# Kernel optimization log

Hardware: AMD Instinct MI355X
Metric: run time of the kernel (lower is better)

Reference implementation:

```python
import jax, jax.numpy as jnp
import numpy as np

B, IN, H, OUT, E = 4096, 1024, 2048, 1024, 16

def setup_inputs() -> dict:
    key = jax.random.key(0)
    ks = jax.random.split(key, 8)
    def lin_init(k, shape, fan_in):
        bound = 1.0 / np.sqrt(fan_in)
        return jax.random.uniform(k, shape, jnp.float32, -bound, bound)
    return {
        "obs": jax.random.normal(ks[0], (B, IN), jnp.float32),
        "switch_idx": jax.random.randint(ks[1], (B,), 0, E, jnp.int32),
        "pre_w": lin_init(ks[2], (H, IN), IN),
        "pre_b": lin_init(ks[3], (H,), IN),
        "expert_w": lin_init(ks[4], (E, H, H), H),
        "expert_b": lin_init(ks[5], (E, H), H),
        "post_w": lin_init(ks[6], (OUT, H), H),
        "post_b": lin_init(ks[7], (OUT,), H),
    }

def reference(obs, switch_idx, pre_w, pre_b, expert_w, expert_b, post_w, post_b):
    # pre_switch: Linear + Tanh
    x = jnp.tanh(obs @ pre_w.T + pre_b)                      # [B, H]
    # compute ALL switch experts (faithful to torch.stack over switches)
    all_x = jnp.einsum("bi,eoi->beo", x, expert_w) + expert_b  # [B, E, H]
    # gather the selected expert output per sample
    x = jnp.take_along_axis(all_x, switch_idx[:, None, None].astype(jnp.int32), axis=1)[:, 0]  # [B, H]
    # post_switch: Tanh, Linear, Tanh
    x = jnp.tanh(x)
    return jnp.tanh(x @ post_w.T + post_b)                   # [B, OUT]
```

## Files before the change

### kernel.cpp

```cpp
#include <hip/hip_runtime.h>


#define Bsz 4096
#define INd 1024
#define Hd  2048
#define OUTd 1024
#define NEXP 16

typedef short bf16x8 __attribute__((ext_vector_type(8)));
typedef float f32x4 __attribute__((ext_vector_type(4)));
typedef unsigned short u16;

__device__ __forceinline__ u16 f2bf(float f) {
  unsigned u = __float_as_uint(f);
  u += 0x7FFF + ((u >> 16) & 1);
  return (u16)(u >> 16);
}

__device__ __forceinline__ float fast_tanh(float x) {
  float ax = fabsf(x);
  float e = __expf(2.0f * ax);
  float t = 1.0f - 2.0f / (e + 1.0f);
  return x < 0.0f ? -t : t;
}

#define GLL16(g, l)                                                            \
  __builtin_amdgcn_global_load_lds(                                            \
      (const __attribute__((address_space(1))) unsigned int*)(g),              \
      (__attribute__((address_space(3))) unsigned int*)(l), 16, 0, 0)

__device__ __forceinline__ void stage128(const u16* gbase, int ldk, u16* lds, int t) {
  const int row = t >> 3;
  const int gc8 = ((t & 7) ^ (row & 7)) << 3;
#pragma unroll
  for (int p = 0; p < 4; ++p)
    GLL16(gbase + (size_t)(row + 32 * p) * ldk + gc8, lds + ((t + 256 * p) << 3));
}

__device__ __forceinline__ void stage64(const u16* gbase, int ldk, u16* lds, int t) {
  const int row = t >> 3;
  const int gc8 = ((t & 7) ^ (row & 7)) << 3;
#pragma unroll
  for (int p = 0; p < 2; ++p)
    GLL16(gbase + (size_t)(row + 32 * p) * ldk + gc8, lds + ((t + 256 * p) << 3));
}

__device__ __forceinline__ void stage_gather(const u16* X1k, const int rowg[4],
                                             const u16* zeroc, u16* lds, int t) {
  const int gc8 = ((t & 7) ^ ((t >> 3) & 7)) << 3;
#pragma unroll
  for (int p = 0; p < 4; ++p) {
    const u16* g = (rowg[p] >= 0) ? X1k + (size_t)rowg[p] * Hd + gc8 : zeroc;
    GLL16(g, lds + ((t + 256 * p) << 3));
  }
}

struct F32Tile { float4 v[8]; };
__device__ __forceinline__ void loadF32tile(const float* W, int ldk, int t, F32Tile& r) {
  const int brow = t & 127, half = t >> 7;
  const float* p = W + (size_t)brow * ldk + (half << 5);
#pragma unroll
  for (int q = 0; q < 8; ++q) r.v[q] = *(const float4*)(p + 4 * q);
}
__device__ __forceinline__ void writeF32tile(const F32Tile& r, u16* lds, int t) {
  const int brow = t & 127, half = t >> 7;
#pragma unroll
  for (int q2 = 0; q2 < 4; ++q2) {
    const float4 x = r.v[2 * q2], y = r.v[2 * q2 + 1];
    bf16x8 o;
    o[0] = (short)f2bf(x.x); o[1] = (short)f2bf(x.y);
    o[2] = (short)f2bf(x.z); o[3] = (short)f2bf(x.w);
    o[4] = (short)f2bf(y.x); o[5] = (short)f2bf(y.y);
    o[6] = (short)f2bf(y.z); o[7] = (short)f2bf(y.w);
    const int gq = (half << 2) + q2;
    const int c = gq ^ (brow & 7);
    *(bf16x8*)&lds[brow * 64 + (c << 3)] = o;
  }
}

template <int MI>
__device__ __forceinline__ void compute_tile(const u16* As, const u16* Bs,
                                             int wm, int wn, int fr, int fq,
                                             f32x4 (&acc)[MI][4]) {
#pragma unroll
  for (int ks = 0; ks < 2; ++ks) {
    const int ch = (((ks << 2) + fq) ^ (fr & 7)) << 3;
    bf16x8 af[MI], bq[4];
#pragma unroll
    for (int i = 0; i < MI; ++i) af[i] = *(const bf16x8*)&As[(wm + 16 * i + fr) * 64 + ch];
#pragma unroll
    for (int j = 0; j < 4; ++j) bq[j] = *(const bf16x8*)&Bs[(wn + 16 * j + fr) * 64 + ch];
#pragma unroll
    for (int i = 0; i < MI; ++i)
#pragma unroll
      for (int j = 0; j < 4; ++j)
        acc[i][j] = __builtin_amdgcn_mfma_f32_16x16x32_bf16(af[i], bq[j], acc[i][j], 0, 0, 0);
  }
}

__global__ __launch_bounds__(256) void k_bucket(const int* __restrict__ idx,
                                                int* __restrict__ offs,
                                                int* __restrict__ rows,
                                                int* __restrict__ zc) {
  __shared__ int cnt[NEXP];
  __shared__ int base[NEXP];
  int t = threadIdx.x;
  if (t < 16) zc[t] = 0;
  if (t < NEXP) cnt[t] = 0;
  __syncthreads();
  for (int b = t; b < Bsz; b += 256) atomicAdd(&cnt[idx[b]], 1);
  __syncthreads();
  if (t == 0) {
    int s = 0;
    for (int e = 0; e < NEXP; ++e) { base[e] = s; offs[e] = s; s += cnt[e]; }
    offs[NEXP] = s;
  }
  __syncthreads();
  for (int b = t; b < Bsz; b += 256) {
    int e = idx[b];
    int p = atomicAdd(&base[e], 1);
    rows[p] = b;
  }
}

__global__ __launch_bounds__(256) void k_cvt(const float* __restrict__ src,
                                             u16* __restrict__ dst, int n) {
  int i = (blockIdx.x * 256 + threadIdx.x) * 8;
  if (i >= n) return;
  float4 a = *(const float4*)(src + i);
  float4 b = *(const float4*)(src + i + 4);
  bf16x8 o;
  o[0] = (short)f2bf(a.x); o[1] = (short)f2bf(a.y);
  o[2] = (short)f2bf(a.z); o[3] = (short)f2bf(a.w);
  o[4] = (short)f2bf(b.x); o[5] = (short)f2bf(b.y);
  o[6] = (short)f2bf(b.z); o[7] = (short)f2bf(b.w);
  *(bf16x8*)(dst + i) = o;
}

template <bool PC>
__global__ __launch_bounds__(256) void k_pre_t(const float* __restrict__ obs32,
                                               const u16* __restrict__ obsb,
                                               const float* __restrict__ prew32,
                                               const u16* __restrict__ prewb,
                                               const float* __restrict__ pre_b,
                                               u16* __restrict__ X1) {
  __shared__ u16 As[2][128 * 64];
  __shared__ u16 Bs[2][128 * 64];
  const int tid = threadIdx.x, lane = tid & 63, wv = tid >> 6;
  const int wm = (wv >> 1) << 6, wn = (wv & 1) << 6;
  const int fr = lane & 15, fq = lane >> 4;
  const int n0 = blockIdx.x * 128, m0 = blockIdx.y * 128;
  f32x4 acc[4][4] = {};
  const int NT = INd / 64;

  if constexpr (PC) {
    stage128(obsb + (size_t)m0 * INd, INd, As[0], tid);
    stage128(prewb + (size_t)n0 * INd, INd, Bs[0], tid);
    __syncthreads();
    for (int kt = 0; kt < NT; ++kt) {
      const int nb = (kt + 1) & 1;
      if (kt + 1 < NT) {
        stage128(obsb + (size_t)m0 * INd + (kt + 1) * 64, INd, As[nb], tid);
        stage128(prewb + (size_t)n0 * INd + (kt + 1) * 64, INd, Bs[nb], tid);
      }
      compute_tile<4>(As[kt & 1], Bs[kt & 1], wm, wn, fr, fq, acc);
      __syncthreads();
    }
  } else {
    F32Tile ra, rb;
    loadF32tile(obs32 + (size_t)m0 * INd, INd, tid, ra);
    loadF32tile(prew32 + (size_t)n0 * INd, INd, tid, rb);
    writeF32tile(ra, As[0], tid);
    writeF32tile(rb, Bs[0], tid);
    __syncthreads();
    for (int kt = 0; kt < NT; ++kt) {
      const int nb = (kt + 1) & 1;
      const bool more = (kt + 1) < NT;
      F32Tile na, nbv;
      if (more) {
        loadF32tile(obs32 + (size_t)m0 * INd + (kt + 1) * 64, INd, tid, na);
        loadF32tile(prew32 + (size_t)n0 * INd + (kt + 1) * 64, INd, tid, nbv);
      }
      compute_tile<4>(As[kt & 1], Bs[kt & 1], wm, wn, fr, fq, acc);
      if (more) { writeF32tile(na, As[nb], tid); writeF32tile(nbv, Bs[nb], tid); }
      __syncthreads();
    }
  }

#pragma unroll
  for (int j = 0; j < 4; ++j) {
    int col = n0 + wn + 16 * j + fr;
    float bias = pre_b[col];
#pragma unroll
    for (int i = 0; i < 4; ++i) {
      int rb2 = m0 + wm + 16 * i + fq * 4;
#pragma unroll
      for (int r = 0; r < 4; ++r)
        X1[(size_t)(rb2 + r) * Hd + col] = f2bf(fast_tanh(acc[i][j][r] + bias));
    }
  }
}

template <bool PC>
__global__ __launch_bounds__(256) void k_expert_t(const u16* __restrict__ X1,
                                                  const float* __restrict__ ew32,
                                                  const u16* __restrict__ ewb,
                                                  const float* __restrict__ eb,
                                                  const int* __restrict__ offs,
                                                  const int* __restrict__ rows,
                                                  const u16* __restrict__ zeroc,
                                                  u16* __restrict__ Z) {
  const int e = blockIdx.y >> 5, rt = blockIdx.y & 31;
  const int seg = offs[e], cnt = offs[e + 1] - seg;
  const int tbase = rt * 128;
  if (tbase >= cnt) return;
  const int nval = min(128, cnt - tbase);
  const int n0 = blockIdx.x * 128;

  __shared__ u16 As[2][128 * 64];
  __shared__ u16 Bs[2][128 * 64];
  const int tid = threadIdx.x, lane = tid & 63, wv = tid >> 6;
  const int wm = (wv >> 1) << 6, wn = (wv & 1) << 6;
  const int fr = lane & 15, fq = lane >> 4;

  int rowg[4];
  {
    const int r0 = tid >> 3;
#pragma unroll
    for (int p = 0; p < 4; ++p) {
      int ar = r0 + 32 * p;
      rowg[p] = (ar < nval) ? rows[seg + tbase + ar] : -1;
    }
  }
  f32x4 acc[4][4] = {};
  const int NT = Hd / 64;

  if constexpr (PC) {
    const u16* We = ewb + (size_t)e * Hd * Hd + (size_t)n0 * Hd;
    stage_gather(X1, rowg, zeroc, As[0], tid);
    stage128(We, Hd, Bs[0], tid);
    __syncthreads();
    for (int kt = 0; kt < NT; ++kt) {
      const int nb = (kt + 1) & 1;
      if (kt + 1 < NT) {
        stage_gather(X1 + (kt + 1) * 64, rowg, zeroc, As[nb], tid);
        stage128(We + (kt + 1) * 64, Hd, Bs[nb], tid);
      }
      compute_tile<4>(As[kt & 1], Bs[kt & 1], wm, wn, fr, fq, acc);
      __syncthreads();
    }
  } else {
    const float* We32 = ew32 + (size_t)e * Hd * Hd + (size_t)n0 * Hd;
    stage_gather(X1, rowg, zeroc, As[0], tid);
    {
      F32Tile rb;
      loadF32tile(We32, Hd, tid, rb);
      writeF32tile(rb, Bs[0], tid);
    }
    __syncthreads();
    for (int kt = 0; kt < NT; ++kt) {
      const int nb = (kt + 1) & 1;
      const bool more = (kt + 1) < NT;
      F32Tile rn;
      if (more) {
        stage_gather(X1 + (kt + 1) * 64, rowg, zeroc, As[nb], tid);
        loadF32tile(We32 + (kt + 1) * 64, Hd, tid, rn);
      }
      compute_tile<4>(As[kt & 1], Bs[kt & 1], wm, wn, fr, fq, acc);
      if (more) writeF32tile(rn, Bs[nb], tid);
      __syncthreads();
    }
  }

#pragma unroll
  for (int i = 0; i < 4; ++i) {
#pragma unroll
    for (int r = 0; r < 4; ++r) {
      int arow = wm + 16 * i + fq * 4 + r;
      if (arow < nval) {
        int orow = rows[seg + tbase + arow];
#pragma unroll
        for (int j = 0; j < 4; ++j) {
          int col = n0 + wn + 16 * j + fr;
          float bias = eb[(size_t)e * Hd + col];
          Z[(size_t)orow * Hd + col] = f2bf(fast_tanh(acc[i][j][r] + bias));
        }
      }
    }
  }
}

template <bool PC>
__global__ __launch_bounds__(256) void k_post_t(const u16* __restrict__ Z,
                                                const float* __restrict__ pw32,
                                                const u16* __restrict__ pwb,
                                                const float* __restrict__ pb,
                                                float* __restrict__ out) {
  __shared__ u16 As[2][64 * 64];
  __shared__ u16 Bs[2][128 * 64];
  const int tid = threadIdx.x, lane = tid & 63, wv = tid >> 6;
  const int wm = (wv >> 1) << 5, wn = (wv & 1) << 6;
  const int fr = lane & 15, fq = lane >> 4;
  const int n0 = blockIdx.x * 128, m0 = blockIdx.y * 64;
  f32x4 acc[2][4] = {};
  const int NT = Hd / 64;

  if constexpr (PC) {
    stage64(Z + (size_t)m0 * Hd, Hd, As[0], tid);
    stage128(pwb + (size_t)n0 * Hd, Hd, Bs[0], tid);
    __syncthreads();
    for (int kt = 0; kt < NT; ++kt) {
      const int nb = (kt + 1) & 1;
      if (kt + 1 < NT) {
        stage64(Z + (size_t)m0 * Hd + (kt + 1) * 64, Hd, As[nb], tid);
        stage128(pwb + (size_t)n0 * Hd + (kt + 1) * 64, Hd, Bs[nb], tid);
      }
      compute_tile<2>(As[kt & 1], Bs[kt & 1], wm, wn, fr, fq, acc);
      __syncthreads();
    }
  } else {
    stage64(Z + (size_t)m0 * Hd, Hd, As[0], tid);
    {
      F32Tile rb;
      loadF32tile(pw32 + (size_t)n0 * Hd, Hd, tid, rb);
      writeF32tile(rb, Bs[0], tid);
    }
    __syncthreads();
    for (int kt = 0; kt < NT; ++kt) {
      const int nb = (kt + 1) & 1;
      const bool more = (kt + 1) < NT;
      F32Tile rn;
      if (more) {
        stage64(Z + (size_t)m0 * Hd + (kt + 1) * 64, Hd, As[nb], tid);
        loadF32tile(pw32 + (size_t)n0 * Hd + (kt + 1) * 64, Hd, tid, rn);
      }
      compute_tile<2>(As[kt & 1], Bs[kt & 1], wm, wn, fr, fq, acc);
      if (more) writeF32tile(rn, Bs[nb], tid);
      __syncthreads();
    }
  }

#pragma unroll
  for (int j = 0; j < 4; ++j) {
    int col = n0 + wn + 16 * j + fr;
    float bias = pb[col];
#pragma unroll
    for (int i = 0; i < 2; ++i) {
      int rb2 = m0 + wm + 16 * i + fq * 4;
#pragma unroll
      for (int r = 0; r < 4; ++r)
        out[(size_t)(rb2 + r) * OUTd + col] = fast_tanh(acc[i][j][r] + bias);
    }
  }
}

extern "C" void kernel_launch(void* const* d_in, const int* in_sizes, int n_in,
                              void* d_out, int out_size, void* d_ws, size_t ws_size,
                              hipStream_t stream) {
  const float* obs   = (const float*)d_in[0];
  const int*   sw    = (const int*)d_in[1];
  const float* pre_w = (const float*)d_in[2];
  const float* pre_b = (const float*)d_in[3];
  const float* ew    = (const float*)d_in[4];
  const float* eb    = (const float*)d_in[5];
  const float* pw    = (const float*)d_in[6];
  const float* pb    = (const float*)d_in[7];
  float* out = (float*)d_out;

  char* ws = (char*)d_ws;
  int* offs = (int*)ws;
  int* rows = (int*)(ws + 128);
  u16* zeroc = (u16*)(ws + 128 + 16384);
  const size_t MISC = 65536;
  u16* X1     = (u16*)(ws + MISC);
  u16* Zb     = (u16*)(ws + MISC + ((size_t)16 << 20));
  u16* obsb   = (u16*)(ws + MISC + ((size_t)32 << 20));
  u16* prewb  = (u16*)(ws + MISC + ((size_t)40 << 20));
  u16* postwb = (u16*)(ws + MISC + ((size_t)44 << 20));
  u16* ewb    = (u16*)(ws + MISC + ((size_t)48 << 20));
  const size_t needMid  = MISC + ((size_t)48 << 20);
  const size_t needFull = needMid + ((size_t)128 << 20);
  const bool full = ws_size >= needFull;
  const bool mid  = ws_size >= needMid;

  k_bucket<<<dim3(1), dim3(256), 0, stream>>>(sw, offs, rows, (int*)zeroc);

  if (mid) {
    k_cvt<<<dim3(Bsz * INd / 2048), dim3(256), 0, stream>>>(obs, obsb, Bsz * INd);
    k_cvt<<<dim3(Hd * INd / 2048), dim3(256), 0, stream>>>(pre_w, prewb, Hd * INd);
    k_cvt<<<dim3(OUTd * Hd / 2048), dim3(256), 0, stream>>>(pw, postwb, OUTd * Hd);
  }
  if (full)
    k_cvt<<<dim3(NEXP * Hd * Hd / 2048), dim3(256), 0, stream>>>(ew, ewb, NEXP * Hd * Hd);

  if (mid)
    k_pre_t<true><<<dim3(Hd / 128, Bsz / 128), dim3(256), 0, stream>>>(obs, obsb, pre_w, prewb, pre_b, X1);
  else
    k_pre_t<false><<<dim3(Hd / 128, Bsz / 128), dim3(256), 0, stream>>>(obs, obsb, pre_w, prewb, pre_b, X1);

  if (full)
    k_expert_t<true><<<dim3(Hd / 128, NEXP * 32), dim3(256), 0, stream>>>(X1, ew, ewb, eb, offs, rows, zeroc, Zb);
  else
    k_expert_t<false><<<dim3(Hd / 128, NEXP * 32), dim3(256), 0, stream>>>(X1, ew, ewb, eb, offs, rows, zeroc, Zb);

  if (mid)
    k_post_t<true><<<dim3(OUTd / 128, Bsz / 64), dim3(256), 0, stream>>>(Zb, pw, postwb, pb, out);
  else
    k_post_t<false><<<dim3(OUTd / 128, Bsz / 64), dim3(256), 0, stream>>>(Zb, pw, postwb, pb, out);
}
```

Baseline: 630.0 us.

## Drop expert weight pre-conversion, fuse bucketing with bf16 casts into one kernel

Removes the separate full conversion of the 16 expert weight matrices to bf16. The expert kernel now always reads fp32 weights and converts them in registers while staging to shared memory. The single-block bucketing kernel is replaced by a small init kernel plus a prep kernel that does a per-expert atomic row scatter (fixed stride per expert) and the bf16 casts of obs, pre_w and post_w in one launch. This avoids writing and re-reading about 128 MB of bf16 expert weights and cuts launch count. In exchange the expert GEMM loads twice the bytes per weight tile, and row order within an expert is now nondeterministic.

Result: no change. 618.3 us (-1.9%).

```diff
diff --git a/kernel.cpp b/kernel.cpp
--- a/kernel.cpp
+++ b/kernel.cpp
@@ -98,43 +98,46 @@
   }
 }
 
-__global__ __launch_bounds__(256) void k_bucket(const int* __restrict__ idx,
-                                                int* __restrict__ offs,
-                                                int* __restrict__ rows,
-                                                int* __restrict__ zc) {
-  __shared__ int cnt[NEXP];
-  __shared__ int base[NEXP];
+__global__ __launch_bounds__(64) void k_init(int* __restrict__ cnt, int* __restrict__ zc) {
   int t = threadIdx.x;
+  if (t < NEXP) cnt[t] = 0;
   if (t < 16) zc[t] = 0;
-  if (t < NEXP) cnt[t] = 0;
-  __syncthreads();
-  for (int b = t; b < Bsz; b += 256) atomicAdd(&cnt[idx[b]], 1);
-  __syncthreads();
-  if (t == 0) {
-    int s = 0;
-    for (int e = 0; e < NEXP; ++e) { base[e] = s; offs[e] = s; s += cnt[e]; }
-    offs[NEXP] = s;
-  }
-  __syncthreads();
-  for (int b = t; b < Bsz; b += 256) {
-    int e = idx[b];
-    int p = atomicAdd(&base[e], 1);
-    rows[p] = b;
-  }
-}
-
-__global__ __launch_bounds__(256) void k_cvt(const float* __restrict__ src,
-                                             u16* __restrict__ dst, int n) {
-  int i = (blockIdx.x * 256 + threadIdx.x) * 8;
-  if (i >= n) return;
-  float4 a = *(const float4*)(src + i);
-  float4 b = *(const float4*)(src + i + 4);
-  bf16x8 o;
-  o[0] = (short)f2bf(a.x); o[1] = (short)f2bf(a.y);
-  o[2] = (short)f2bf(a.z); o[3] = (short)f2bf(a.w);
-  o[4] = (short)f2bf(b.x); o[5] = (short)f2bf(b.y);
-  o[6] = (short)f2bf(b.z); o[7] = (short)f2bf(b.w);
-  *(bf16x8*)(dst + i) = o;
+}
+
+__global__ __launch_bounds__(256) void k_prep(const int* __restrict__ sw,
+                                              int* __restrict__ cnt,
+                                              int* __restrict__ rows,
+                                              const float* __restrict__ obs,  u16* __restrict__ obsb,
+                                              const float* __restrict__ prew, u16* __restrict__ prewb,
+                                              const float* __restrict__ pw,   u16* __restrict__ postwb,
+                                              int docvt) {
+  const int bid = blockIdx.x, tid = threadIdx.x;
+  if (bid < 16) {
+    const int r = bid * 256 + tid;
+    const int e = sw[r];
+    const int p = atomicAdd(&cnt[e], 1);
+    rows[e * Bsz + p] = r;
+    return;
+  }
+  if (!docvt) return;
+  const int c0 = bid - 16;
+#pragma unroll
+  for (int q = 0; q < 2; ++q) {
+    const int c = c0 + q * 2048;
+    const float* src; u16* dst;
+    if (c < 2048)      { src = obs  + (size_t)c * 2048;          dst = obsb   + (size_t)c * 2048; }
+    else if (c < 3072) { src = prew + (size_t)(c - 2048) * 2048; dst = prewb  + (size_t)(c - 2048) * 2048; }
+    else               { src = pw   + (size_t)(c - 3072) * 2048; dst = postwb + (size_t)(c - 3072) * 2048; }
+    const int i = tid * 8;
+    float4 a = *(const float4*)(src + i);
+    float4 b = *(const float4*)(src + i + 4);
+    bf16x8 o;
+    o[0] = (short)f2bf(a.x); o[1] = (short)f2bf(a.y);
+    o[2] = (short)f2bf(a.z); o[3] = (short)f2bf(a.w);
+    o[4] = (short)f2bf(b.x); o[5] = (short)f2bf(b.y);
+    o[6] = (short)f2bf(b.z); o[7] = (short)f2bf(b.w);
+    *(bf16x8*)(dst + i) = o;
+  }
 }
 
 template <bool PC>
@@ -201,21 +204,20 @@
   }
 }
 
-template <bool PC>
-__global__ __launch_bounds__(256) void k_expert_t(const u16* __restrict__ X1,
-                                                  const float* __restrict__ ew32,
-                                                  const u16* __restrict__ ewb,
-                                                  const float* __restrict__ eb,
-                                                  const int* __restrict__ offs,
-                                                  const int* __restrict__ rows,
-                                                  const u16* __restrict__ zeroc,
-                                                  u16* __restrict__ Z) {
+__global__ __launch_bounds__(256) void k_expert(const u16* __restrict__ X1,
+                                                const float* __restrict__ ew32,
+                                                const float* __restrict__ eb,
+                                                const int* __restrict__ cnt,
+                                                const int* __restrict__ rows,
+                                                const u16* __restrict__ zeroc,
+                                                u16* __restrict__ Z) {
   const int e = blockIdx.y >> 5, rt = blockIdx.y & 31;
-  const int seg = offs[e], cnt = offs[e + 1] - seg;
+  const int ce = cnt[e];
   const int tbase = rt * 128;
-  if (tbase >= cnt) return;
-  const int nval = min(128, cnt - tbase);
+  if (tbase >= ce) return;
+  const int nval = min(128, ce - tbase);
   const int n0 = blockIdx.x * 128;
+  const int* rowsE = rows + e * Bsz + tbase;
 
   __shared__ u16 As[2][128 * 64];
   __shared__ u16 Bs[2][128 * 64];
@@ -229,48 +231,36 @@
 #pragma unroll
     for (int p = 0; p < 4; ++p) {
       int ar = r0 + 32 * p;
-      rowg[p] = (ar < nval) ? rows[seg + tbase + ar] : -1;
+      rowg[p] = (ar < nval) ? rowsE[ar] : -1;
     }
   }
   f32x4 acc[4][4] = {};
   const int NT = Hd / 64;
 
-  if constexpr (PC) {
-    const u16* We = ewb + (size_t)e * Hd * Hd + (size_t)n0 * Hd;
-    stage_gather(X1, rowg, zeroc, As[0], tid);
-    stage128(We, Hd, Bs[0], tid);
-    __syncthreads();
-    for (int kt = 0; kt < NT; ++kt) {
-      const int nb = (kt + 1) & 1;
-      if (kt + 1 < NT) {
-        stage_gather(X1 + (kt + 1) * 64, rowg, zeroc, As[nb], tid);
-        stage128(We + (kt + 1) * 64, Hd, Bs[nb], tid);
-      }
-      compute_tile<4>(As[kt & 1], Bs[kt & 1], wm, wn, fr, fq, acc);
-      __syncthreads();
-    }
-  } else {
-    const float* We32 = ew32 + (size_t)e * Hd * Hd + (size_t)n0 * Hd;
-    stage_gather(X1, rowg, zeroc, As[0], tid);
-    {
-      F32Tile rb;
-      loadF32tile(We32, Hd, tid, rb);
-      writeF32tile(rb, Bs[0], tid);
-    }
-    __syncthreads();
-    for (int kt = 0; kt < NT; ++kt) {
-      const int nb = (kt + 1) & 1;
-      const bool more = (kt + 1) < NT;
-      F32Tile rn;
-      if (more) {
-        stage_gather(X1 + (kt + 1) * 64, rowg, zeroc, As[nb], tid);
-        loadF32tile(We32 + (kt + 1) * 64, Hd, tid, rn);
-      }
-      compute_tile<4>(As[kt & 1], Bs[kt & 1], wm, wn, fr, fq, acc);
-      if (more) writeF32tile(rn, Bs[nb], tid);
-      __syncthreads();
-    }
-  }
+  const float* We32 = ew32 + (size_t)e * Hd * Hd + (size_t)n0 * Hd;
+  stage_gather(X1, rowg, zeroc, As[0], tid);
+  {
+    F32Tile rb;
+    loadF32tile(We32, Hd, tid, rb);
+    writeF32tile(rb, Bs[0], tid);
+  }
+  __syncthreads();
+  for (int kt = 0; kt < NT; ++kt) {
+    const int nb = (kt + 1) & 1;
+    const bool more = (kt + 1) < NT;
+    F32Tile rn;
+    if (more) {
+      stage_gather(X1 + (kt + 1) * 64, rowg, zeroc, As[nb], tid);
+      loadF32tile(We32 + (kt + 1) * 64, Hd, tid, rn);
+    }
+    compute_tile<4>(As[kt & 1], Bs[kt & 1], wm, wn, fr, fq, acc);
+    if (more) writeF32tile(rn, Bs[nb], tid);
+    __syncthreads();
+  }
+
+  float bias[4];
+#pragma unroll
+  for (int j = 0; j < 4; ++j) bias[j] = eb[(size_t)e * Hd + n0 + wn + 16 * j + fr];
 
 #pragma unroll
   for (int i = 0; i < 4; ++i) {
@@ -278,12 +268,11 @@
     for (int r = 0; r < 4; ++r) {
       int arow = wm + 16 * i + fq * 4 + r;
       if (arow < nval) {
-        int orow = rows[seg + tbase + arow];
+        int orow = rowsE[arow];
 #pragma unroll
         for (int j = 0; j < 4; ++j) {
           int col = n0 + wn + 16 * j + fr;
-          float bias = eb[(size_t)e * Hd + col];
-          Z[(size_t)orow * Hd + col] = f2bf(fast_tanh(acc[i][j][r] + bias));
+          Z[(size_t)orow * Hd + col] = f2bf(fast_tanh(acc[i][j][r] + bias[j]));
         }
       }
     }
@@ -368,42 +357,30 @@
   float* out = (float*)d_out;
 
   char* ws = (char*)d_ws;
-  int* offs = (int*)ws;
-  int* rows = (int*)(ws + 128);
-  u16* zeroc = (u16*)(ws + 128 + 16384);
-  const size_t MISC = 65536;
-  u16* X1     = (u16*)(ws + MISC);
-  u16* Zb     = (u16*)(ws + MISC + ((size_t)16 << 20));
-  u16* obsb   = (u16*)(ws + MISC + ((size_t)32 << 20));
-  u16* prewb  = (u16*)(ws + MISC + ((size_t)40 << 20));
-  u16* postwb = (u16*)(ws + MISC + ((size_t)44 << 20));
-  u16* ewb    = (u16*)(ws + MISC + ((size_t)48 << 20));
-  const size_t needMid  = MISC + ((size_t)48 << 20);
-  const size_t needFull = needMid + ((size_t)128 << 20);
-  const bool full = ws_size >= needFull;
-  const bool mid  = ws_size >= needMid;
-
-  k_bucket<<<dim3(1), dim3(256), 0, stream>>>(sw, offs, rows, (int*)zeroc);
-
-  if (mid) {
-    k_cvt<<<dim3(Bsz * INd / 2048), dim3(256), 0, stream>>>(obs, obsb, Bsz * INd);
-    k_cvt<<<dim3(Hd * INd / 2048), dim3(256), 0, stream>>>(pre_w, prewb, Hd * INd);
-    k_cvt<<<dim3(OUTd * Hd / 2048), dim3(256), 0, stream>>>(pw, postwb, OUTd * Hd);
-  }
-  if (full)
-    k_cvt<<<dim3(NEXP * Hd * Hd / 2048), dim3(256), 0, stream>>>(ew, ewb, NEXP * Hd * Hd);
-
-  if (mid)
+  int* cnt  = (int*)ws;
+  int* zc   = (int*)(ws + 256);
+  int* rows = (int*)(ws + 4096);
+  const size_t M1 = (size_t)1 << 20;
+  u16* X1     = (u16*)(ws + M1);
+  u16* Zb     = (u16*)(ws + M1 + ((size_t)16 << 20));
+  u16* obsb   = (u16*)(ws + M1 + ((size_t)32 << 20));
+  u16* prewb  = (u16*)(ws + M1 + ((size_t)40 << 20));
+  u16* postwb = (u16*)(ws + M1 + ((size_t)44 << 20));
+  const bool pc = ws_size >= M1 + ((size_t)48 << 20);
+
+  k_init<<<dim3(1), dim3(64), 0, stream>>>(cnt, zc);
+
+  k_prep<<<dim3(pc ? 2064 : 16), dim3(256), 0, stream>>>(
+      sw, cnt, rows, obs, obsb, pre_w, prewb, pw, postwb, pc ? 1 : 0);
+
+  if (pc)
     k_pre_t<true><<<dim3(Hd / 128, Bsz / 128), dim3(256), 0, stream>>>(obs, obsb, pre_w, prewb, pre_b, X1);
   else
     k_pre_t<false><<<dim3(Hd / 128, Bsz / 128), dim3(256), 0, stream>>>(obs, obsb, pre_w, prewb, pre_b, X1);
 
-  if (full)
-    k_expert_t<true><<<dim3(Hd / 128, NEXP * 32), dim3(256), 0, stream>>>(X1, ew, ewb, eb, offs, rows, zeroc, Zb);
-  else
-    k_expert_t<false><<<dim3(Hd / 128, NEXP * 32), dim3(256), 0, stream>>>(X1, ew, ewb, eb, offs, rows, zeroc, Zb);
-
-  if (mid)
+  k_expert<<<dim3(Hd / 128, NEXP * 32), dim3(256), 0, stream>>>(X1, ew, eb, cnt, rows, (const u16*)zc, Zb);
+
+  if (pc)
     k_post_t<true><<<dim3(OUTd / 128, Bsz / 64), dim3(256), 0, stream>>>(Zb, pw, postwb, pb, out);
   else
     k_post_t<false><<<dim3(OUTd / 128, Bsz / 64), dim3(256), 0, stream>>>(Zb, pw, postwb, pb, out);
```
